# Performance work log

Measured on AMD Instinct MI355X. Metric: run time of the kernel, lower is better.

Reference implementation:

```python
import jax, jax.numpy as jnp
import numpy as np

B, D_IN, NQ, H = 65536, 385, 64, 16  # batch, input dim, num questions, head width
DIMS = [385, 512, 256, 192]


def setup_inputs() -> dict:
    key = jax.random.key(0)
    ks = jax.random.split(key, 12)
    s = 0.02
    inp = {
        "x": jax.random.normal(ks[0], (B, D_IN), jnp.float32),
        "W1": jax.random.normal(ks[1], (DIMS[0], DIMS[1]), jnp.float32) * s,
        "b1": jnp.zeros((DIMS[1],), jnp.float32),
        "W2": jax.random.normal(ks[2], (DIMS[1], DIMS[2]), jnp.float32) * s,
        "b2": jnp.zeros((DIMS[2],), jnp.float32),
        "W3": jax.random.normal(ks[3], (DIMS[2], DIMS[3]), jnp.float32) * s,
        "b3": jnp.zeros((DIMS[3],), jnp.float32),
        # all true/false heads stacked: layout [qid, correct, H] flattened on last axis
        "Wh": jax.random.normal(ks[4], (DIMS[3], NQ * 2 * H), jnp.float32) * s,
        "bh": jnp.zeros((NQ * 2 * H,), jnp.float32),
        "question_ids": jax.random.randint(ks[5], (B,), 0, NQ, jnp.int32),
        "is_correct": jax.random.randint(ks[6], (B,), 0, 2, jnp.int32),
    }
    return inp


def reference(x, W1, b1, W2, b2, W3, b3, Wh, bh, question_ids, is_correct):
    # shared trunk (dropout is identity at eval); activation = relu
    h = jax.nn.relu(x @ W1 + b1)          # [B, 512]
    h = jax.nn.relu(h @ W2 + b2)          # [B, 256]
    h = jax.nn.relu(h @ W3 + b3)          # [B, 192] shared features
    # compute all heads densely, then gather the per-row head slice —
    # equivalent to routing each row to its (question_id, is_correct) Linear head
    logits_all = h @ Wh + bh              # [B, NQ*2*H]
    base = (question_ids * 2 + is_correct) * H        # [B]
    idx = base[:, None] + jnp.arange(H)[None, :]      # [B, H]
    return jnp.take_along_axis(logits_all, idx, axis=1)  # [B, H]
```

## Files before the change

kernel.cpp:

```cpp
#include <hip/hip_runtime.h>
#include <hip/hip_bf16.h>

#define THREADS 1024
#define ROWS 128

typedef __attribute__((ext_vector_type(4))) float f32x4;
typedef __attribute__((ext_vector_type(8))) short s16x8;

__device__ __forceinline__ unsigned short bfbits(float f) {
  __bf16 h = (__bf16)f;
  return __builtin_bit_cast(unsigned short, h);
}
__device__ __forceinline__ float bf2f(unsigned short h) {
  unsigned u = ((unsigned)h) << 16;
  return __builtin_bit_cast(float, u);
}

__global__ void prep_kernel(const float* __restrict__ W1, const float* __restrict__ W2,
                            const float* __restrict__ W3, const float* __restrict__ Wh,
                            unsigned short* __restrict__ w1f, unsigned short* __restrict__ w2f,
                            unsigned short* __restrict__ w3f, unsigned short* __restrict__ whT) {
  int u = blockIdx.x * blockDim.x + threadIdx.x;
  const int U1 = 24576, U2 = 16384, U3 = 6144, U4 = 49152;
  if (u < U1) {
    int lane = u & 63, r = (u >> 6) & 31, c = u >> 11;
    int f  = r * 16 + (lane & 15);
    int kb = c * 32 + ((lane >> 4) << 3);
    s16x8 v;
    #pragma unroll
    for (int j = 0; j < 8; ++j) v[j] = (short)bfbits(W1[(kb + j) * 512 + f]);
    *(s16x8*)(w1f + (u << 3)) = v;
    return;
  }
  u -= U1;
  if (u < U2) {
    int lane = u & 63, r = (u >> 6) & 15, c = u >> 10;
    int f  = r * 16 + (lane & 15);
    int kb = c * 32 + ((lane >> 4) << 3);
    s16x8 v;
    #pragma unroll
    for (int j = 0; j < 8; ++j) v[j] = (short)bfbits(W2[(kb + j) * 256 + f]);
    *(s16x8*)(w2f + (u << 3)) = v;
    return;
  }
  u -= U2;
  if (u < U3) {
    int lane = u & 63, t = u >> 6;
    int c = t / 12, r = t - c * 12;
    int f  = r * 16 + (lane & 15);
    int kb = c * 32 + ((lane >> 4) << 3);
    s16x8 v;
    #pragma unroll
    for (int j = 0; j < 8; ++j) v[j] = (short)bfbits(W3[(kb + j) * 192 + f]);
    *(s16x8*)(w3f + (u << 3)) = v;
    return;
  }
  u -= U3;
  if (u < U4) {
    int j = u & 15, v2 = u >> 4;
    int fo = v2 % 24, head = v2 / 24;
    s16x8 v;
    #pragma unroll
    for (int i = 0; i < 8; ++i) v[i] = (short)bfbits(Wh[(fo * 8 + i) * 2048 + head * 16 + j]);
    *(s16x8*)(whT + u * 8) = v;
  }
}

#define MFMA(a, b, c) __builtin_amdgcn_mfma_f32_16x16x32_bf16((a), (b), (c), 0, 0, 0)
#define SWZ(lp) (((lp) * 16) ^ ((((lp) >> 4) & 3) << 5))

#define G1_RANGE(P, C0, C1)                                                          \
  _Pragma("unroll")                                                                  \
  for (int c = (C0); c < (C1); ++c) {                                                \
    s16x8 af = *(const s16x8*)(w1f + (((c * 32 + (P) * 16 + w) * 64 + lane) << 3));  \
    _Pragma("unroll")                                                                \
    for (int bt = 0; bt < 8; ++bt) {                                                 \
      s16x8 bfr = *(const s16x8*)(xall + (c << 13) + (bt << 10) + swz_l);            \
      acc1[bt] = MFMA(af, bfr, acc1[bt]);                                            \
    }                                                                                \
  }

__global__ __launch_bounds__(THREADS, 4)
void fused_mlp(const float* __restrict__ x,
               const float* __restrict__ b1,
               const float* __restrict__ b2,
               const float* __restrict__ b3,
               const float* __restrict__ bh,
               const float* __restrict__ W1,
               const int* __restrict__ qid,
               const int* __restrict__ corr,
               const unsigned short* __restrict__ w1f,
               const unsigned short* __restrict__ w2f,
               const unsigned short* __restrict__ w3f,
               const unsigned short* __restrict__ whT,
               float* __restrict__ out) {
  __shared__ __align__(16) unsigned char lds[163840];
  unsigned char*  xall = lds;
  unsigned char*  hL   = lds;
  unsigned short* h3b  = (unsigned short*)lds;
  unsigned char*  hH   = lds + 98304;
  unsigned char*  h2f  = lds + 98304;

  const int tid  = threadIdx.x;
  const int lane = tid & 63;
  const int w    = tid >> 6;
  const int b0   = blockIdx.x * ROWS;
  const int l15  = lane & 15;
  const int lh   = lane >> 4;
  const int swz_l = SWZ(lane);

  const int s_wi  = tid & 511;
  const int s_ci  = tid >> 9;
  const int s_bt  = s_wi >> 6;
  const int s_lp  = s_wi & 63;
  const float* s_base = x + (size_t)(b0 + (s_bt << 4) + (s_lp & 15)) * 385 + ((s_lp >> 4) << 3);
  const int s_abase = (s_bt << 10) + SWZ(s_lp);

  f32x4 sv0, sv1;
  auto sload = [&](int g) {
    int c = (g << 1) + s_ci;
    sv0 = *(const f32x4*)(s_base + c * 32);
    sv1 = *(const f32x4*)(s_base + c * 32 + 4);
  };
  auto swrite = [&](int g) {
    int c = (g << 1) + s_ci;
    s16x8 v;
    v[0] = (short)bfbits(sv0[0]); v[1] = (short)bfbits(sv0[1]);
    v[2] = (short)bfbits(sv0[2]); v[3] = (short)bfbits(sv0[3]);
    v[4] = (short)bfbits(sv1[0]); v[5] = (short)bfbits(sv1[1]);
    v[6] = (short)bfbits(sv1[2]); v[7] = (short)bfbits(sv1[3]);
    *(s16x8*)(xall + (c << 13) + s_abase) = v;
  };

  f32x4 acc1[8];
  #pragma unroll
  for (int bt = 0; bt < 8; ++bt) acc1[bt] = (f32x4)0.0f;

  auto epi1 = [&](int P, unsigned char* dst) {
    int fg = P * 256 + w * 16 + lh * 4;
    f32x4 bv = *(const f32x4*)(b1 + fg);
    f32x4 wv = *(const f32x4*)(W1 + 384 * 512 + fg);
    int so = ((w >> 1) << 13) + SWZ(l15 + (((2 * w + (lh >> 1)) & 3) << 4)) + ((lh & 1) << 3);
    #pragma unroll
    for (int bt = 0; bt < 8; ++bt) {
      float xv = x[(size_t)(b0 + (bt << 4) + l15) * 385 + 384];
      float v0 = fmaxf(acc1[bt][0] + bv[0] + wv[0] * xv, 0.f);
      float v1 = fmaxf(acc1[bt][1] + bv[1] + wv[1] * xv, 0.f);
      float v2 = fmaxf(acc1[bt][2] + bv[2] + wv[2] * xv, 0.f);
      float v3 = fmaxf(acc1[bt][3] + bv[3] + wv[3] * xv, 0.f);
      unsigned plo = (unsigned)bfbits(v0) | ((unsigned)bfbits(v1) << 16);
      unsigned phi = (unsigned)bfbits(v2) | ((unsigned)bfbits(v3) << 16);
      unsigned long long pk = (unsigned long long)plo | ((unsigned long long)phi << 32);
      *(unsigned long long*)(dst + so + (bt << 10)) = pk;
      acc1[bt] = (f32x4)0.0f;
    }
  };

  sload(0); swrite(0);
  __syncthreads();

  sload(1); G1_RANGE(0, 0, 2)  swrite(1); __syncthreads();
  sload(2); G1_RANGE(0, 2, 4)  swrite(2); __syncthreads();
  sload(3); G1_RANGE(0, 4, 6)  swrite(3); __syncthreads();
  sload(4); G1_RANGE(0, 6, 8)  swrite(4); __syncthreads();
  sload(5); G1_RANGE(0, 8, 10) swrite(5); __syncthreads();

  G1_RANGE(0, 10, 12)
  epi1(0, hH);

  G1_RANGE(1, 0, 12)
  __syncthreads();
  epi1(1, hL);
  __syncthreads();

  f32x4 acc2[8];
  #pragma unroll
  for (int bt = 0; bt < 8; ++bt) acc2[bt] = (f32x4)0.0f;

  #pragma unroll
  for (int c = 0; c < 8; ++c) {
    s16x8 a2 = *(const s16x8*)(w2f + (((c * 16 + w) * 64 + lane) << 3));
    #pragma unroll
    for (int bt = 0; bt < 8; ++bt) {
      s16x8 bfr = *(const s16x8*)(hH + (c << 13) + (bt << 10) + swz_l);
      acc2[bt] = MFMA(a2, bfr, acc2[bt]);
    }
  }
  #pragma unroll
  for (int c = 8; c < 16; ++c) {
    s16x8 a2 = *(const s16x8*)(w2f + (((c * 16 + w) * 64 + lane) << 3));
    #pragma unroll
    for (int bt = 0; bt < 8; ++bt) {
      s16x8 bfr = *(const s16x8*)(hL + ((c - 8) << 13) + (bt << 10) + swz_l);
      acc2[bt] = MFMA(a2, bfr, acc2[bt]);
    }
  }
  __syncthreads();

  {
    int fg = w * 16 + lh * 4;
    f32x4 bv = *(const f32x4*)(b2 + fg);
    int so = ((w >> 1) << 13) + SWZ(l15 + (((2 * w + (lh >> 1)) & 3) << 4)) + ((lh & 1) << 3);
    #pragma unroll
    for (int bt = 0; bt < 8; ++bt) {
      float v0 = fmaxf(acc2[bt][0] + bv[0], 0.f);
      float v1 = fmaxf(acc2[bt][1] + bv[1], 0.f);
      float v2 = fmaxf(acc2[bt][2] + bv[2], 0.f);
      float v3 = fmaxf(acc2[bt][3] + bv[3], 0.f);
      unsigned plo = (unsigned)bfbits(v0) | ((unsigned)bfbits(v1) << 16);
      unsigned phi = (unsigned)bfbits(v2) | ((unsigned)bfbits(v3) << 16);
      unsigned long long pk = (unsigned long long)plo | ((unsigned long long)phi << 32);
      *(unsigned long long*)(h2f + so + (bt << 10)) = pk;
    }
  }
  __syncthreads();

  const int hrow = tid >> 4, hj = tid & 15;
  const int head0 = qid[b0 + hrow] * 2 + corr[b0 + hrow];
  const int head1 = qid[b0 + 64 + hrow] * 2 + corr[b0 + 64 + hrow];

  if (w < 12) {
    f32x4 acc3[8];
    #pragma unroll
    for (int bt = 0; bt < 8; ++bt) acc3[bt] = (f32x4)0.0f;
    #pragma unroll
    for (int c = 0; c < 8; ++c) {
      s16x8 a3 = *(const s16x8*)(w3f + (((c * 12 + w) * 64 + lane) << 3));
      #pragma unroll
      for (int bt = 0; bt < 8; ++bt) {
        s16x8 bfr = *(const s16x8*)(h2f + (c << 13) + (bt << 10) + swz_l);
        acc3[bt] = MFMA(a3, bfr, acc3[bt]);
      }
    }
    int fg = w * 16 + lh * 4;
    f32x4 bv = *(const f32x4*)(b3 + fg);
    #pragma unroll
    for (int bt = 0; bt < 8; ++bt) {
      int row = (bt << 4) + l15;
      float v0 = fmaxf(acc3[bt][0] + bv[0], 0.f);
      float v1 = fmaxf(acc3[bt][1] + bv[1], 0.f);
      float v2 = fmaxf(acc3[bt][2] + bv[2], 0.f);
      float v3 = fmaxf(acc3[bt][3] + bv[3], 0.f);
      unsigned plo = (unsigned)bfbits(v0) | ((unsigned)bfbits(v1) << 16);
      unsigned phi = (unsigned)bfbits(v2) | ((unsigned)bfbits(v3) << 16);
      unsigned long long pk = (unsigned long long)plo | ((unsigned long long)phi << 32);
      *(unsigned long long*)((unsigned char*)h3b + row * 400 + w * 32 + lh * 8) = pk;
    }
  }
  __syncthreads();

  #pragma unroll
  for (int q = 0; q < 2; ++q) {
    int row  = q * 64 + hrow;
    int head = q ? head1 : head0;
    const unsigned short* wp = whT + ((head * 24) * 16 + hj) * 8;
    const unsigned short* hp = h3b + row * 200;
    float acc = bh[(head << 4) + hj];
    #pragma unroll 6
    for (int fo = 0; fo < 24; ++fo) {
      s16x8 wv = *(const s16x8*)(wp + fo * 128);
      s16x8 hv = *(const s16x8*)(hp + fo * 8);
      #pragma unroll
      for (int e = 0; e < 8; ++e)
        acc += bf2f((unsigned short)wv[e]) * bf2f((unsigned short)hv[e]);
    }
    out[(size_t)(b0 + row) * 16 + hj] = acc;
  }
}

extern "C" void kernel_launch(void* const* d_in, const int* in_sizes, int n_in,
                              void* d_out, int out_size, void* d_ws, size_t ws_size,
                              hipStream_t stream) {
  (void)in_sizes; (void)n_in; (void)out_size; (void)ws_size;
  const float* x  = (const float*)d_in[0];
  const float* W1 = (const float*)d_in[1];
  const float* b1 = (const float*)d_in[2];
  const float* W2 = (const float*)d_in[3];
  const float* b2 = (const float*)d_in[4];
  const float* W3 = (const float*)d_in[5];
  const float* b3 = (const float*)d_in[6];
  const float* Wh = (const float*)d_in[7];
  const float* bh = (const float*)d_in[8];
  const int* qid  = (const int*)d_in[9];
  const int* corr = (const int*)d_in[10];
  float* out = (float*)d_out;

  unsigned short* w1f = (unsigned short*)d_ws;
  unsigned short* w2f = w1f + 12 * 32 * 64 * 8;
  unsigned short* w3f = w2f + 16 * 16 * 64 * 8;
  unsigned short* whT = w3f + 8 * 12 * 64 * 8;

  prep_kernel<<<376, 256, 0, stream>>>(W1, W2, W3, Wh, w1f, w2f, w3f, whT);
  fused_mlp<<<65536 / ROWS, THREADS, 0, stream>>>(x, b1, b2, b3, bh, W1, qid, corr,
                                                  w1f, w2f, w3f, whT, out);
}
```

Measured before the change: 103.4 us.

## Halve block to 64 rows and 8 waves, each wave computing two feature tiles

Shrinks each block from 128 rows and 16 waves to 64 rows and 8 waves, with LDS halved to 80KB so more blocks can be resident per CU. Each wave now computes two 16-feature tiles per B-fragment read, reusing the LDS B operand across two MFMAs. Layer 3 is rebalanced so all 8 waves participate, with waves 0-3 taking an extra tile. The trade-off is twice as many blocks, so per-block weight fragment loads are repeated more often.

```diff
diff --git a/kernel.cpp b/kernel.cpp
--- a/kernel.cpp
+++ b/kernel.cpp
@@ -1,8 +1,8 @@
 #include <hip/hip_runtime.h>
 #include <hip/hip_bf16.h>
 
-#define THREADS 1024
-#define ROWS 128
+#define THREADS 512
+#define ROWS 64
 
 typedef __attribute__((ext_vector_type(4))) float f32x4;
 typedef __attribute__((ext_vector_type(8))) short s16x8;
@@ -69,15 +69,17 @@
 #define MFMA(a, b, c) __builtin_amdgcn_mfma_f32_16x16x32_bf16((a), (b), (c), 0, 0, 0)
 #define SWZ(lp) (((lp) * 16) ^ ((((lp) >> 4) & 3) << 5))
 
-#define G1_RANGE(P, C0, C1)                                                          \
-  _Pragma("unroll")                                                                  \
-  for (int c = (C0); c < (C1); ++c) {                                                \
-    s16x8 af = *(const s16x8*)(w1f + (((c * 32 + (P) * 16 + w) * 64 + lane) << 3));  \
-    _Pragma("unroll")                                                                \
-    for (int bt = 0; bt < 8; ++bt) {                                                 \
-      s16x8 bfr = *(const s16x8*)(xall + (c << 13) + (bt << 10) + swz_l);            \
-      acc1[bt] = MFMA(af, bfr, acc1[bt]);                                            \
-    }                                                                                \
+#define G1_RANGE(P, C0, C1)                                                                 \
+  _Pragma("unroll")                                                                         \
+  for (int c = (C0); c < (C1); ++c) {                                                       \
+    s16x8 a0 = *(const s16x8*)(w1f + (((c * 32 + (P) * 16 + w * 2 + 0) * 64 + lane) << 3)); \
+    s16x8 a1 = *(const s16x8*)(w1f + (((c * 32 + (P) * 16 + w * 2 + 1) * 64 + lane) << 3)); \
+    _Pragma("unroll")                                                                       \
+    for (int bt = 0; bt < 4; ++bt) {                                                        \
+      s16x8 bfr = *(const s16x8*)(xall + (c << 12) + (bt << 10) + swz_l);                   \
+      acc1[0][bt] = MFMA(a0, bfr, acc1[0][bt]);                                             \
+      acc1[1][bt] = MFMA(a1, bfr, acc1[1][bt]);                                             \
+    }                                                                                       \
   }
 
 __global__ __launch_bounds__(THREADS, 4)
@@ -94,12 +96,12 @@
                const unsigned short* __restrict__ w3f,
                const unsigned short* __restrict__ whT,
                float* __restrict__ out) {
-  __shared__ __align__(16) unsigned char lds[163840];
+  __shared__ __align__(16) unsigned char lds[81920];
   unsigned char*  xall = lds;
-  unsigned char*  hL   = lds;
+  unsigned char*  h1L  = lds;
   unsigned short* h3b  = (unsigned short*)lds;
-  unsigned char*  hH   = lds + 98304;
-  unsigned char*  h2f  = lds + 98304;
+  unsigned char*  h1H  = lds + 49152;
+  unsigned char*  h2f  = lds + 49152;
 
   const int tid  = threadIdx.x;
   const int lane = tid & 63;
@@ -109,10 +111,10 @@
   const int lh   = lane >> 4;
   const int swz_l = SWZ(lane);
 
-  const int s_wi  = tid & 511;
-  const int s_ci  = tid >> 9;
-  const int s_bt  = s_wi >> 6;
-  const int s_lp  = s_wi & 63;
+  const int s_ci = tid >> 8;
+  const int s_wi = tid & 255;
+  const int s_bt = s_wi >> 6;
+  const int s_lp = s_wi & 63;
   const float* s_base = x + (size_t)(b0 + (s_bt << 4) + (s_lp & 15)) * 385 + ((s_lp >> 4) << 3);
   const int s_abase = (s_bt << 10) + SWZ(s_lp);
 
@@ -129,30 +131,36 @@
     v[2] = (short)bfbits(sv0[2]); v[3] = (short)bfbits(sv0[3]);
     v[4] = (short)bfbits(sv1[0]); v[5] = (short)bfbits(sv1[1]);
     v[6] = (short)bfbits(sv1[2]); v[7] = (short)bfbits(sv1[3]);
-    *(s16x8*)(xall + (c << 13) + s_abase) = v;
+    *(s16x8*)(xall + (c << 12) + s_abase) = v;
   };
 
-  f32x4 acc1[8];
-  #pragma unroll
-  for (int bt = 0; bt < 8; ++bt) acc1[bt] = (f32x4)0.0f;
+  f32x4 acc1[2][4];
+  #pragma unroll
+  for (int a = 0; a < 2; ++a)
+    #pragma unroll
+    for (int bt = 0; bt < 4; ++bt) acc1[a][bt] = (f32x4)0.0f;
 
   auto epi1 = [&](int P, unsigned char* dst) {
-    int fg = P * 256 + w * 16 + lh * 4;
-    f32x4 bv = *(const f32x4*)(b1 + fg);
-    f32x4 wv = *(const f32x4*)(W1 + 384 * 512 + fg);
-    int so = ((w >> 1) << 13) + SWZ(l15 + (((2 * w + (lh >> 1)) & 3) << 4)) + ((lh & 1) << 3);
-    #pragma unroll
-    for (int bt = 0; bt < 8; ++bt) {
-      float xv = x[(size_t)(b0 + (bt << 4) + l15) * 385 + 384];
-      float v0 = fmaxf(acc1[bt][0] + bv[0] + wv[0] * xv, 0.f);
-      float v1 = fmaxf(acc1[bt][1] + bv[1] + wv[1] * xv, 0.f);
-      float v2 = fmaxf(acc1[bt][2] + bv[2] + wv[2] * xv, 0.f);
-      float v3 = fmaxf(acc1[bt][3] + bv[3] + wv[3] * xv, 0.f);
-      unsigned plo = (unsigned)bfbits(v0) | ((unsigned)bfbits(v1) << 16);
-      unsigned phi = (unsigned)bfbits(v2) | ((unsigned)bfbits(v3) << 16);
-      unsigned long long pk = (unsigned long long)plo | ((unsigned long long)phi << 32);
-      *(unsigned long long*)(dst + so + (bt << 10)) = pk;
-      acc1[bt] = (f32x4)0.0f;
+    #pragma unroll
+    for (int a = 0; a < 2; ++a) {
+      int ft = w * 2 + a;
+      int fg = P * 256 + (ft << 4) + (lh << 2);
+      f32x4 bv = *(const f32x4*)(b1 + fg);
+      f32x4 wv = *(const f32x4*)(W1 + 384 * 512 + fg);
+      int so = ((ft >> 1) << 12) + SWZ(l15 + ((((ft & 1) << 1) + (lh >> 1)) << 4)) + ((lh & 1) << 3);
+      #pragma unroll
+      for (int bt = 0; bt < 4; ++bt) {
+        float xv = x[(size_t)(b0 + (bt << 4) + l15) * 385 + 384];
+        float v0 = fmaxf(acc1[a][bt][0] + bv[0] + wv[0] * xv, 0.f);
+        float v1 = fmaxf(acc1[a][bt][1] + bv[1] + wv[1] * xv, 0.f);
+        float v2 = fmaxf(acc1[a][bt][2] + bv[2] + wv[2] * xv, 0.f);
+        float v3 = fmaxf(acc1[a][bt][3] + bv[3] + wv[3] * xv, 0.f);
+        unsigned plo = (unsigned)bfbits(v0) | ((unsigned)bfbits(v1) << 16);
+        unsigned phi = (unsigned)bfbits(v2) | ((unsigned)bfbits(v3) << 16);
+        unsigned long long pk = (unsigned long long)plo | ((unsigned long long)phi << 32);
+        *(unsigned long long*)(dst + so + (bt << 10)) = pk;
+        acc1[a][bt] = (f32x4)0.0f;
+      }
     }
   };
 
@@ -166,47 +174,46 @@
   sload(5); G1_RANGE(0, 8, 10) swrite(5); __syncthreads();
 
   G1_RANGE(0, 10, 12)
-  epi1(0, hH);
+  epi1(0, h1H);
 
   G1_RANGE(1, 0, 12)
   __syncthreads();
-  epi1(1, hL);
-  __syncthreads();
-
-  f32x4 acc2[8];
-  #pragma unroll
-  for (int bt = 0; bt < 8; ++bt) acc2[bt] = (f32x4)0.0f;
-
-  #pragma unroll
-  for (int c = 0; c < 8; ++c) {
-    s16x8 a2 = *(const s16x8*)(w2f + (((c * 16 + w) * 64 + lane) << 3));
-    #pragma unroll
-    for (int bt = 0; bt < 8; ++bt) {
-      s16x8 bfr = *(const s16x8*)(hH + (c << 13) + (bt << 10) + swz_l);
-      acc2[bt] = MFMA(a2, bfr, acc2[bt]);
-    }
-  }
-  #pragma unroll
-  for (int c = 8; c < 16; ++c) {
-    s16x8 a2 = *(const s16x8*)(w2f + (((c * 16 + w) * 64 + lane) << 3));
-    #pragma unroll
-    for (int bt = 0; bt < 8; ++bt) {
-      s16x8 bfr = *(const s16x8*)(hL + ((c - 8) << 13) + (bt << 10) + swz_l);
-      acc2[bt] = MFMA(a2, bfr, acc2[bt]);
-    }
-  }
-  __syncthreads();
-
-  {
-    int fg = w * 16 + lh * 4;
+  epi1(1, h1L);
+  __syncthreads();
+
+  f32x4 acc2[2][4];
+  #pragma unroll
+  for (int i = 0; i < 2; ++i)
+    #pragma unroll
+    for (int bt = 0; bt < 4; ++bt) acc2[i][bt] = (f32x4)0.0f;
+
+  #pragma unroll
+  for (int c = 0; c < 16; ++c) {
+    const unsigned char* reg = (c < 8) ? h1H : h1L;
+    int cl = c & 7;
+    s16x8 a20 = *(const s16x8*)(w2f + (((c * 16 + w * 2 + 0) * 64 + lane) << 3));
+    s16x8 a21 = *(const s16x8*)(w2f + (((c * 16 + w * 2 + 1) * 64 + lane) << 3));
+    #pragma unroll
+    for (int bt = 0; bt < 4; ++bt) {
+      s16x8 bfr = *(const s16x8*)(reg + (cl << 12) + (bt << 10) + swz_l);
+      acc2[0][bt] = MFMA(a20, bfr, acc2[0][bt]);
+      acc2[1][bt] = MFMA(a21, bfr, acc2[1][bt]);
+    }
+  }
+  __syncthreads();
+
+  #pragma unroll
+  for (int i = 0; i < 2; ++i) {
+    int ft = w * 2 + i;
+    int fg = (ft << 4) + (lh << 2);
     f32x4 bv = *(const f32x4*)(b2 + fg);
-    int so = ((w >> 1) << 13) + SWZ(l15 + (((2 * w + (lh >> 1)) & 3) << 4)) + ((lh & 1) << 3);
-    #pragma unroll
-    for (int bt = 0; bt < 8; ++bt) {
-      float v0 = fmaxf(acc2[bt][0] + bv[0], 0.f);
-      float v1 = fmaxf(acc2[bt][1] + bv[1], 0.f);
-      float v2 = fmaxf(acc2[bt][2] + bv[2], 0.f);
-      float v3 = fmaxf(acc2[bt][3] + bv[3], 0.f);
+    int so = ((ft >> 1) << 12) + SWZ(l15 + ((((ft & 1) << 1) + (lh >> 1)) << 4)) + ((lh & 1) << 3);
+    #pragma unroll
+    for (int bt = 0; bt < 4; ++bt) {
+      float v0 = fmaxf(acc2[i][bt][0] + bv[0], 0.f);
+      float v1 = fmaxf(acc2[i][bt][1] + bv[1], 0.f);
+      float v2 = fmaxf(acc2[i][bt][2] + bv[2], 0.f);
+      float v3 = fmaxf(acc2[i][bt][3] + bv[3], 0.f);
       unsigned plo = (unsigned)bfbits(v0) | ((unsigned)bfbits(v1) << 16);
       unsigned phi = (unsigned)bfbits(v2) | ((unsigned)bfbits(v3) << 16);
       unsigned long long pk = (unsigned long long)plo | ((unsigned long long)phi << 32);
@@ -217,41 +224,53 @@
 
   const int hrow = tid >> 4, hj = tid & 15;
   const int head0 = qid[b0 + hrow] * 2 + corr[b0 + hrow];
-  const int head1 = qid[b0 + 64 + hrow] * 2 + corr[b0 + 64 + hrow];
-
-  if (w < 12) {
-    f32x4 acc3[8];
-    #pragma unroll
-    for (int bt = 0; bt < 8; ++bt) acc3[bt] = (f32x4)0.0f;
+  const int head1 = qid[b0 + 32 + hrow] * 2 + corr[b0 + 32 + hrow];
+
+  {
+    f32x4 acc3[2][4];
+    #pragma unroll
+    for (int i = 0; i < 2; ++i)
+      #pragma unroll
+      for (int bt = 0; bt < 4; ++bt) acc3[i][bt] = (f32x4)0.0f;
+
     #pragma unroll
     for (int c = 0; c < 8; ++c) {
-      s16x8 a3 = *(const s16x8*)(w3f + (((c * 12 + w) * 64 + lane) << 3));
+      s16x8 a30 = *(const s16x8*)(w3f + (((c * 12 + w) * 64 + lane) << 3));
+      s16x8 a31;
+      if (w < 4) a31 = *(const s16x8*)(w3f + (((c * 12 + 8 + w) * 64 + lane) << 3));
       #pragma unroll
-      for (int bt = 0; bt < 8; ++bt) {
-        s16x8 bfr = *(const s16x8*)(h2f + (c << 13) + (bt << 10) + swz_l);
-        acc3[bt] = MFMA(a3, bfr, acc3[bt]);
+      for (int bt = 0; bt < 4; ++bt) {
+        s16x8 bfr = *(const s16x8*)(h2f + (c << 12) + (bt << 10) + swz_l);
+        acc3[0][bt] = MFMA(a30, bfr, acc3[0][bt]);
+        if (w < 4) acc3[1][bt] = MFMA(a31, bfr, acc3[1][bt]);
       }
     }
-    int fg = w * 16 + lh * 4;
-    f32x4 bv = *(const f32x4*)(b3 + fg);
-    #pragma unroll
-    for (int bt = 0; bt < 8; ++bt) {
-      int row = (bt << 4) + l15;
-      float v0 = fmaxf(acc3[bt][0] + bv[0], 0.f);
-      float v1 = fmaxf(acc3[bt][1] + bv[1], 0.f);
-      float v2 = fmaxf(acc3[bt][2] + bv[2], 0.f);
-      float v3 = fmaxf(acc3[bt][3] + bv[3], 0.f);
-      unsigned plo = (unsigned)bfbits(v0) | ((unsigned)bfbits(v1) << 16);
-      unsigned phi = (unsigned)bfbits(v2) | ((unsigned)bfbits(v3) << 16);
-      unsigned long long pk = (unsigned long long)plo | ((unsigned long long)phi << 32);
-      *(unsigned long long*)((unsigned char*)h3b + row * 400 + w * 32 + lh * 8) = pk;
+    #pragma unroll
+    for (int i = 0; i < 2; ++i) {
+      if (i == 0 || w < 4) {
+        int ft = (i == 0) ? w : (8 + w);
+        int fg = (ft << 4) + (lh << 2);
+        f32x4 bv = *(const f32x4*)(b3 + fg);
+        #pragma unroll
+        for (int bt = 0; bt < 4; ++bt) {
+          int row = (bt << 4) + l15;
+          float v0 = fmaxf(acc3[i][bt][0] + bv[0], 0.f);
+          float v1 = fmaxf(acc3[i][bt][1] + bv[1], 0.f);
+          float v2 = fmaxf(acc3[i][bt][2] + bv[2], 0.f);
+          float v3 = fmaxf(acc3[i][bt][3] + bv[3], 0.f);
+          unsigned plo = (unsigned)bfbits(v0) | ((unsigned)bfbits(v1) << 16);
+          unsigned phi = (unsigned)bfbits(v2) | ((unsigned)bfbits(v3) << 16);
+          unsigned long long pk = (unsigned long long)plo | ((unsigned long long)phi << 32);
+          *(unsigned long long*)((unsigned char*)h3b + row * 400 + (ft << 5) + (lh << 3)) = pk;
+        }
+      }
     }
   }
   __syncthreads();
 
   #pragma unroll
   for (int q = 0; q < 2; ++q) {
-    int row  = q * 64 + hrow;
+    int row  = q * 32 + hrow;
     int head = q ? head1 : head0;
     const unsigned short* wp = whT + ((head * 24) * 16 + hj) * 8;
     const unsigned short* hp = h3b + row * 200;
```

New measurement: 92.43 us. 1.12x faster.

## Restructure fused MLP to 64-row blocks with x fragments held in registers

Applied to the files above, without the earlier changes.

Halves the block to 512 threads over 64 rows and cuts LDS from 160KB to 64KB so more blocks can be resident per CU. Each wave now owns a 16-row tile and keeps its bf16 x fragments in registers instead of staging them through LDS with a pipelined load loop. Weight fragments are now reloaded from global/L2 for each 16-row tile rather than being shared across 8 row tiles per wave. This trades more weight traffic and lower MFMA reuse per A-fragment for higher occupancy and fewer barriers.

```diff
diff --git a/kernel.cpp b/kernel.cpp
--- a/kernel.cpp
+++ b/kernel.cpp
@@ -1,8 +1,8 @@
 #include <hip/hip_runtime.h>
 #include <hip/hip_bf16.h>
 
-#define THREADS 1024
-#define ROWS 128
+#define THREADS 512
+#define ROWS 64
 
 typedef __attribute__((ext_vector_type(4))) float f32x4;
 typedef __attribute__((ext_vector_type(8))) short s16x8;
@@ -68,17 +68,6 @@
 
 #define MFMA(a, b, c) __builtin_amdgcn_mfma_f32_16x16x32_bf16((a), (b), (c), 0, 0, 0)
 #define SWZ(lp) (((lp) * 16) ^ ((((lp) >> 4) & 3) << 5))
-
-#define G1_RANGE(P, C0, C1)                                                          \
-  _Pragma("unroll")                                                                  \
-  for (int c = (C0); c < (C1); ++c) {                                                \
-    s16x8 af = *(const s16x8*)(w1f + (((c * 32 + (P) * 16 + w) * 64 + lane) << 3));  \
-    _Pragma("unroll")                                                                \
-    for (int bt = 0; bt < 8; ++bt) {                                                 \
-      s16x8 bfr = *(const s16x8*)(xall + (c << 13) + (bt << 10) + swz_l);            \
-      acc1[bt] = MFMA(af, bfr, acc1[bt]);                                            \
-    }                                                                                \
-  }
 
 __global__ __launch_bounds__(THREADS, 4)
 void fused_mlp(const float* __restrict__ x,
@@ -94,167 +83,125 @@
                const unsigned short* __restrict__ w3f,
                const unsigned short* __restrict__ whT,
                float* __restrict__ out) {
-  __shared__ __align__(16) unsigned char lds[163840];
-  unsigned char*  xall = lds;
-  unsigned char*  hL   = lds;
-  unsigned short* h3b  = (unsigned short*)lds;
-  unsigned char*  hH   = lds + 98304;
-  unsigned char*  h2f  = lds + 98304;
+  __shared__ __align__(16) unsigned char lds[65536];
 
   const int tid  = threadIdx.x;
   const int lane = tid & 63;
   const int w    = tid >> 6;
+  const int rt   = w & 3;
+  const int fh   = w >> 2;
   const int b0   = blockIdx.x * ROWS;
   const int l15  = lane & 15;
   const int lh   = lane >> 4;
   const int swz_l = SWZ(lane);
-
-  const int s_wi  = tid & 511;
-  const int s_ci  = tid >> 9;
-  const int s_bt  = s_wi >> 6;
-  const int s_lp  = s_wi & 63;
-  const float* s_base = x + (size_t)(b0 + (s_bt << 4) + (s_lp & 15)) * 385 + ((s_lp >> 4) << 3);
-  const int s_abase = (s_bt << 10) + SWZ(s_lp);
-
-  f32x4 sv0, sv1;
-  auto sload = [&](int g) {
-    int c = (g << 1) + s_ci;
-    sv0 = *(const f32x4*)(s_base + c * 32);
-    sv1 = *(const f32x4*)(s_base + c * 32 + 4);
-  };
-  auto swrite = [&](int g) {
-    int c = (g << 1) + s_ci;
-    s16x8 v;
-    v[0] = (short)bfbits(sv0[0]); v[1] = (short)bfbits(sv0[1]);
-    v[2] = (short)bfbits(sv0[2]); v[3] = (short)bfbits(sv0[3]);
-    v[4] = (short)bfbits(sv1[0]); v[5] = (short)bfbits(sv1[1]);
-    v[6] = (short)bfbits(sv1[2]); v[7] = (short)bfbits(sv1[3]);
-    *(s16x8*)(xall + (c << 13) + s_abase) = v;
-  };
-
-  f32x4 acc1[8];
-  #pragma unroll
-  for (int bt = 0; bt < 8; ++bt) acc1[bt] = (f32x4)0.0f;
-
-  auto epi1 = [&](int P, unsigned char* dst) {
-    int fg = P * 256 + w * 16 + lh * 4;
+  const int r0   = b0 + (rt << 4);
+
+  const float* xrow = x + (size_t)(r0 + l15) * 385 + (lh << 3);
+  s16x8 xf[12];
+  #pragma unroll
+  for (int c = 0; c < 12; ++c) {
+    f32x4 lo = *(const f32x4*)(xrow + c * 32);
+    f32x4 hi = *(const f32x4*)(xrow + c * 32 + 4);
+    s16x8 v;
+    v[0] = (short)bfbits(lo[0]); v[1] = (short)bfbits(lo[1]);
+    v[2] = (short)bfbits(lo[2]); v[3] = (short)bfbits(lo[3]);
+    v[4] = (short)bfbits(hi[0]); v[5] = (short)bfbits(hi[1]);
+    v[6] = (short)bfbits(hi[2]); v[7] = (short)bfbits(hi[3]);
+    xf[c] = v;
+  }
+  const float xv384 = x[(size_t)(r0 + l15) * 385 + 384];
+
+  #pragma unroll
+  for (int t = 0; t < 16; ++t) {
+    int ft = (fh << 4) + t;
+    f32x4 acc = (f32x4)0.0f;
+    #pragma unroll
+    for (int c = 0; c < 12; ++c) {
+      s16x8 af = *(const s16x8*)(w1f + (((c * 32 + ft) * 64 + lane) << 3));
+      acc = MFMA(af, xf[c], acc);
+    }
+    int fg = (ft << 4) + (lh << 2);
     f32x4 bv = *(const f32x4*)(b1 + fg);
     f32x4 wv = *(const f32x4*)(W1 + 384 * 512 + fg);
-    int so = ((w >> 1) << 13) + SWZ(l15 + (((2 * w + (lh >> 1)) & 3) << 4)) + ((lh & 1) << 3);
-    #pragma unroll
-    for (int bt = 0; bt < 8; ++bt) {
-      float xv = x[(size_t)(b0 + (bt << 4) + l15) * 385 + 384];
-      float v0 = fmaxf(acc1[bt][0] + bv[0] + wv[0] * xv, 0.f);
-      float v1 = fmaxf(acc1[bt][1] + bv[1] + wv[1] * xv, 0.f);
-      float v2 = fmaxf(acc1[bt][2] + bv[2] + wv[2] * xv, 0.f);
-      float v3 = fmaxf(acc1[bt][3] + bv[3] + wv[3] * xv, 0.f);
-      unsigned plo = (unsigned)bfbits(v0) | ((unsigned)bfbits(v1) << 16);
-      unsigned phi = (unsigned)bfbits(v2) | ((unsigned)bfbits(v3) << 16);
-      unsigned long long pk = (unsigned long long)plo | ((unsigned long long)phi << 32);
-      *(unsigned long long*)(dst + so + (bt << 10)) = pk;
-      acc1[bt] = (f32x4)0.0f;
-    }
-  };
-
-  sload(0); swrite(0);
-  __syncthreads();
-
-  sload(1); G1_RANGE(0, 0, 2)  swrite(1); __syncthreads();
-  sload(2); G1_RANGE(0, 2, 4)  swrite(2); __syncthreads();
-  sload(3); G1_RANGE(0, 4, 6)  swrite(3); __syncthreads();
-  sload(4); G1_RANGE(0, 6, 8)  swrite(4); __syncthreads();
-  sload(5); G1_RANGE(0, 8, 10) swrite(5); __syncthreads();
-
-  G1_RANGE(0, 10, 12)
-  epi1(0, hH);
-
-  G1_RANGE(1, 0, 12)
-  __syncthreads();
-  epi1(1, hL);
-  __syncthreads();
-
-  f32x4 acc2[8];
-  #pragma unroll
-  for (int bt = 0; bt < 8; ++bt) acc2[bt] = (f32x4)0.0f;
-
-  #pragma unroll
-  for (int c = 0; c < 8; ++c) {
-    s16x8 a2 = *(const s16x8*)(w2f + (((c * 16 + w) * 64 + lane) << 3));
-    #pragma unroll
-    for (int bt = 0; bt < 8; ++bt) {
-      s16x8 bfr = *(const s16x8*)(hH + (c << 13) + (bt << 10) + swz_l);
-      acc2[bt] = MFMA(a2, bfr, acc2[bt]);
-    }
-  }
-  #pragma unroll
-  for (int c = 8; c < 16; ++c) {
-    s16x8 a2 = *(const s16x8*)(w2f + (((c * 16 + w) * 64 + lane) << 3));
-    #pragma unroll
-    for (int bt = 0; bt < 8; ++bt) {
-      s16x8 bfr = *(const s16x8*)(hL + ((c - 8) << 13) + (bt << 10) + swz_l);
-      acc2[bt] = MFMA(a2, bfr, acc2[bt]);
-    }
-  }
-  __syncthreads();
-
-  {
-    int fg = w * 16 + lh * 4;
+    float v0 = fmaxf(acc[0] + bv[0] + wv[0] * xv384, 0.f);
+    float v1 = fmaxf(acc[1] + bv[1] + wv[1] * xv384, 0.f);
+    float v2 = fmaxf(acc[2] + bv[2] + wv[2] * xv384, 0.f);
+    float v3 = fmaxf(acc[3] + bv[3] + wv[3] * xv384, 0.f);
+    unsigned plo = (unsigned)bfbits(v0) | ((unsigned)bfbits(v1) << 16);
+    unsigned phi = (unsigned)bfbits(v2) | ((unsigned)bfbits(v3) << 16);
+    unsigned long long pk = (unsigned long long)plo | ((unsigned long long)phi << 32);
+    int khB = ((ft & 1) << 1) + (lh >> 1);
+    int so  = (rt << 14) + ((ft >> 1) << 10) + SWZ(l15 + (khB << 4)) + ((lh & 1) << 3);
+    *(unsigned long long*)(lds + so) = pk;
+  }
+  __syncthreads();
+
+  unsigned long long h2p[8];
+  #pragma unroll
+  for (int t = 0; t < 8; ++t) {
+    int ft2 = (fh << 3) + t;
+    f32x4 acc = (f32x4)0.0f;
+    #pragma unroll
+    for (int c = 0; c < 16; ++c) {
+      s16x8 a2  = *(const s16x8*)(w2f + (((c * 16 + ft2) * 64 + lane) << 3));
+      s16x8 bfr = *(const s16x8*)(lds + (rt << 14) + (c << 10) + swz_l);
+      acc = MFMA(a2, bfr, acc);
+    }
+    int fg = (ft2 << 4) + (lh << 2);
     f32x4 bv = *(const f32x4*)(b2 + fg);
-    int so = ((w >> 1) << 13) + SWZ(l15 + (((2 * w + (lh >> 1)) & 3) << 4)) + ((lh & 1) << 3);
-    #pragma unroll
-    for (int bt = 0; bt < 8; ++bt) {
-      float v0 = fmaxf(acc2[bt][0] + bv[0], 0.f);
-      float v1 = fmaxf(acc2[bt][1] + bv[1], 0.f);
-      float v2 = fmaxf(acc2[bt][2] + bv[2], 0.f);
-      float v3 = fmaxf(acc2[bt][3] + bv[3], 0.f);
-      unsigned plo = (unsigned)bfbits(v0) | ((unsigned)bfbits(v1) << 16);
-      unsigned phi = (unsigned)bfbits(v2) | ((unsigned)bfbits(v3) << 16);
-      unsigned long long pk = (unsigned long long)plo | ((unsigned long long)phi << 32);
-      *(unsigned long long*)(h2f + so + (bt << 10)) = pk;
-    }
+    float v0 = fmaxf(acc[0] + bv[0], 0.f);
+    float v1 = fmaxf(acc[1] + bv[1], 0.f);
+    float v2 = fmaxf(acc[2] + bv[2], 0.f);
+    float v3 = fmaxf(acc[3] + bv[3], 0.f);
+    unsigned plo = (unsigned)bfbits(v0) | ((unsigned)bfbits(v1) << 16);
+    unsigned phi = (unsigned)bfbits(v2) | ((unsigned)bfbits(v3) << 16);
+    h2p[t] = (unsigned long long)plo | ((unsigned long long)phi << 32);
+  }
+  __syncthreads();
+
+  #pragma unroll
+  for (int t = 0; t < 8; ++t) {
+    int ft2 = (fh << 3) + t;
+    int khB = ((ft2 & 1) << 1) + (lh >> 1);
+    int so  = (rt << 13) + ((ft2 >> 1) << 10) + SWZ(l15 + (khB << 4)) + ((lh & 1) << 3);
+    *(unsigned long long*)(lds + so) = h2p[t];
   }
   __syncthreads();
 
   const int hrow = tid >> 4, hj = tid & 15;
   const int head0 = qid[b0 + hrow] * 2 + corr[b0 + hrow];
-  const int head1 = qid[b0 + 64 + hrow] * 2 + corr[b0 + 64 + hrow];
-
-  if (w < 12) {
-    f32x4 acc3[8];
-    #pragma unroll
-    for (int bt = 0; bt < 8; ++bt) acc3[bt] = (f32x4)0.0f;
+  const int head1 = qid[b0 + 32 + hrow] * 2 + corr[b0 + 32 + hrow];
+
+  #pragma unroll
+  for (int t = 0; t < 6; ++t) {
+    int ft3 = fh * 6 + t;
+    f32x4 acc = (f32x4)0.0f;
     #pragma unroll
     for (int c = 0; c < 8; ++c) {
-      s16x8 a3 = *(const s16x8*)(w3f + (((c * 12 + w) * 64 + lane) << 3));
-      #pragma unroll
-      for (int bt = 0; bt < 8; ++bt) {
-        s16x8 bfr = *(const s16x8*)(h2f + (c << 13) + (bt << 10) + swz_l);
-        acc3[bt] = MFMA(a3, bfr, acc3[bt]);
-      }
-    }
-    int fg = w * 16 + lh * 4;
+      s16x8 a3  = *(const s16x8*)(w3f + (((c * 12 + ft3) * 64 + lane) << 3));
+      s16x8 bfr = *(const s16x8*)(lds + (rt << 13) + (c << 10) + swz_l);
+      acc = MFMA(a3, bfr, acc);
+    }
+    int fg = (ft3 << 4) + (lh << 2);
     f32x4 bv = *(const f32x4*)(b3 + fg);
-    #pragma unroll
-    for (int bt = 0; bt < 8; ++bt) {
-      int row = (bt << 4) + l15;
-      float v0 = fmaxf(acc3[bt][0] + bv[0], 0.f);
-      float v1 = fmaxf(acc3[bt][1] + bv[1], 0.f);
-      float v2 = fmaxf(acc3[bt][2] + bv[2], 0.f);
-      float v3 = fmaxf(acc3[bt][3] + bv[3], 0.f);
-      unsigned plo = (unsigned)bfbits(v0) | ((unsigned)bfbits(v1) << 16);
-      unsigned phi = (unsigned)bfbits(v2) | ((unsigned)bfbits(v3) << 16);
-      unsigned long long pk = (unsigned long long)plo | ((unsigned long long)phi << 32);
-      *(unsigned long long*)((unsigned char*)h3b + row * 400 + w * 32 + lh * 8) = pk;
-    }
-  }
-  __syncthreads();
-
+    float v0 = fmaxf(acc[0] + bv[0], 0.f);
+    float v1 = fmaxf(acc[1] + bv[1], 0.f);
+    float v2 = fmaxf(acc[2] + bv[2], 0.f);
+    float v3 = fmaxf(acc[3] + bv[3], 0.f);
+    unsigned plo = (unsigned)bfbits(v0) | ((unsigned)bfbits(v1) << 16);
+    unsigned phi = (unsigned)bfbits(v2) | ((unsigned)bfbits(v3) << 16);
+    unsigned long long pk = (unsigned long long)plo | ((unsigned long long)phi << 32);
+    *(unsigned long long*)(lds + 36864 + rt * 6400 + l15 * 400 + (fg << 1)) = pk;
+  }
+  __syncthreads();
+
+  const unsigned short* h3s = (const unsigned short*)(lds + 36864);
   #pragma unroll
   for (int q = 0; q < 2; ++q) {
-    int row  = q * 64 + hrow;
+    int row  = q * 32 + hrow;
     int head = q ? head1 : head0;
     const unsigned short* wp = whT + ((head * 24) * 16 + hj) * 8;
-    const unsigned short* hp = h3b + row * 200;
+    const unsigned short* hp = h3s + (row >> 4) * 3200 + (row & 15) * 200;
     float acc = bh[(head << 4) + hj];
     #pragma unroll 6
     for (int fo = 0; fo < 24; ++fo) {
@@ -286,9 +233,9 @@
   float* out = (float*)d_out;
 
   unsigned short* w1f = (unsigned short*)d_ws;
-  unsigned short* w2f = w1f + 12 * 32 * 64 * 8;
-  unsigned short* w3f = w2f + 16 * 16 * 64 * 8;
-  unsigned short* whT = w3f + 8 * 12 * 64 * 8;
+  unsigned short* w2f = w1f + 196608;
+  unsigned short* w3f = w2f + 131072;
+  unsigned short* whT = w3f + 49152;
 
   prep_kernel<<<376, 256, 0, stream>>>(W1, W2, W3, Wh, w1f, w2f, w3f, whT);
   fused_mlp<<<65536 / ROWS, THREADS, 0, stream>>>(x, b1, b2, b3, bh, W1, qid, corr,
```

Result: slower. 145.1 us (+40.4%).
